# Kernel tuning notes

Hardware: AMD Instinct MI355X
Metric: run time of the kernel (lower is better)

The kernel has to match this reference:

```python
import jax, jax.numpy as jnp
import numpy as np

B, S, H = 32, 2048, 1024  # S == MAX_LENGTH
SIGMA = 1.0


def setup_inputs() -> dict:
    key = jax.random.key(0)
    k1, k2, k3, k4 = jax.random.split(key, 4)
    return {
        "encoder_outputs": jax.random.normal(k1, (B, S, H), dtype=jnp.float32),
        "decoder_hidden": jax.random.normal(k2, (B, H), dtype=jnp.float32),
        "timestep": jax.random.randint(k3, (B,), 0, S, dtype=jnp.int32),
        # 0.02 scale keeps align scores in a sane range so softmax is not saturated
        "Wa_w": jax.random.normal(k4, (H, H), dtype=jnp.float32) * 0.02,
        "Wa_b": jnp.zeros((H,), dtype=jnp.float32),
    }


def reference(encoder_outputs, decoder_hidden, timestep, Wa_w, Wa_b):
    # method='monotonic', align_method='general'
    b, s_len, h = encoder_outputs.shape

    # align 'general': scores[b,s] = dec[b] . (Wa @ enc[b,s])  (torch Linear: x @ W^T + b)
    keys = jnp.einsum('bsh,dh->bsd', encoder_outputs, Wa_w) + Wa_b  # [B,S,H]
    scores = jnp.einsum('bh,bsh->bs', decoder_hidden, keys)          # [B,S]

    # monotonic: p_t = timestep, gaussian window centered at p_t
    s = jnp.arange(s_len, dtype=jnp.float32)                          # [S]
    p_t = timestep.astype(jnp.float32)[:, None]                       # [B,1]
    gaussian = jnp.exp(-((s[None, :] - p_t) ** 2) / (2.0 * SIGMA ** 2))  # [B,S]

    attn = jax.nn.softmax(scores, axis=1) * gaussian                  # [B,S]
    context = jnp.einsum('bs,bsh->bh', attn, encoder_outputs)         # [B,H]
    return context, attn
```

## Files before the change

### kernel.cpp

```cpp
#include <hip/hip_runtime.h>

#define NB 32
#define NS 2048
#define NH 1024
#define WIN 15

__global__ __launch_bounds__(256) void k1_v(const float* __restrict__ dec,
                                            const float* __restrict__ Wa,
                                            float* __restrict__ v,
                                            double* __restrict__ denomD) {
    __shared__ float4 red4[256];
    int blk = blockIdx.x;
    int b = blk & 31, ht = blk >> 5;
    int t = threadIdx.x;
    if (blk == 0 && t < NB) denomD[t] = 0.0;

    int ds = t >> 6, hl = t & 63;
    int h = ht * 256 + hl * 4;
    const float* decb = dec + b * NH + ds * 256;
    const float* wa   = Wa + (size_t)(ds * 256) * NH + h;

    float4 accA = {0.f, 0.f, 0.f, 0.f}, accB = {0.f, 0.f, 0.f, 0.f};
#pragma unroll 4
    for (int d = 0; d < 256; d += 2) {
        float sA = decb[d];
        float sB = decb[d + 1];
        float4 wA = *(const float4*)(wa + (size_t)d * NH);
        float4 wB = *(const float4*)(wa + (size_t)(d + 1) * NH);
        accA.x = fmaf(sA, wA.x, accA.x); accA.y = fmaf(sA, wA.y, accA.y);
        accA.z = fmaf(sA, wA.z, accA.z); accA.w = fmaf(sA, wA.w, accA.w);
        accB.x = fmaf(sB, wB.x, accB.x); accB.y = fmaf(sB, wB.y, accB.y);
        accB.z = fmaf(sB, wB.z, accB.z); accB.w = fmaf(sB, wB.w, accB.w);
    }
    float4 acc = {accA.x + accB.x, accA.y + accB.y, accA.z + accB.z, accA.w + accB.w};
    red4[t] = acc;
    __syncthreads();
    if (t < 64) {
        float4 r0 = red4[t], r1 = red4[t + 64], r2 = red4[t + 128], r3 = red4[t + 192];
        float4 r = {r0.x + r1.x + r2.x + r3.x, r0.y + r1.y + r2.y + r3.y,
                    r0.z + r1.z + r2.z + r3.z, r0.w + r1.w + r2.w + r3.w};
        *(float4*)(v + b * NH + ht * 256 + t * 4) = r;
    }
}

__global__ __launch_bounds__(512) void k2_scores(const float* __restrict__ enc,
                                                 const float* __restrict__ v,
                                                 float* __restrict__ scores,
                                                 double* __restrict__ denomD) {
    __shared__ float vs[NH];
    __shared__ float rowsc[64];
    int t = threadIdx.x, wid = t >> 6, lane = t & 63;
    int b = blockIdx.x >> 5;
    int row0 = blockIdx.x << 6;

    ((float2*)vs)[t] = ((const float2*)(v + b * NH))[t];
    __syncthreads();
    const float4* vv = (const float4*)vs;
    float4 vr0 = vv[lane], vr1 = vv[64 + lane], vr2 = vv[128 + lane], vr3 = vv[192 + lane];

#pragma unroll
    for (int tile = 0; tile < 2; ++tile) {
        int r0 = row0 + tile * 32 + wid * 4;
        const float4* eb = (const float4*)(enc + (size_t)r0 * NH);
        float acc[4];
#pragma unroll
        for (int r = 0; r < 4; ++r) {
            float4 x0 = eb[r * 256 + lane];
            float4 x1 = eb[r * 256 + 64 + lane];
            float4 x2 = eb[r * 256 + 128 + lane];
            float4 x3 = eb[r * 256 + 192 + lane];
            float s = 0.f;
            s = fmaf(x0.x, vr0.x, s); s = fmaf(x0.y, vr0.y, s);
            s = fmaf(x0.z, vr0.z, s); s = fmaf(x0.w, vr0.w, s);
            s = fmaf(x1.x, vr1.x, s); s = fmaf(x1.y, vr1.y, s);
            s = fmaf(x1.z, vr1.z, s); s = fmaf(x1.w, vr1.w, s);
            s = fmaf(x2.x, vr2.x, s); s = fmaf(x2.y, vr2.y, s);
            s = fmaf(x2.z, vr2.z, s); s = fmaf(x2.w, vr2.w, s);
            s = fmaf(x3.x, vr3.x, s); s = fmaf(x3.y, vr3.y, s);
            s = fmaf(x3.z, vr3.z, s); s = fmaf(x3.w, vr3.w, s);
            acc[r] = s;
        }
#pragma unroll
        for (int r = 0; r < 4; ++r) {
#pragma unroll
            for (int off = 32; off >= 1; off >>= 1) acc[r] += __shfl_xor(acc[r], off, 64);
            if (lane == 0) {
                scores[r0 + r] = acc[r];
                rowsc[tile * 32 + wid * 4 + r] = acc[r];
            }
        }
    }
    __syncthreads();
    if (t < 64) {
        double e = exp((double)rowsc[t]);
#pragma unroll
        for (int off = 32; off >= 1; off >>= 1) e += __shfl_xor(e, off, 64);
        if (t == 0) atomicAdd(&denomD[b], e);
    }
}

__global__ __launch_bounds__(256) void k3_out(const float* __restrict__ enc,
                                              const float* __restrict__ scores,
                                              const int* __restrict__ ts,
                                              const double* __restrict__ denomD,
                                              float* __restrict__ ctx,
                                              float* __restrict__ attn) {
    __shared__ float wv[32];
    int b = blockIdx.x >> 3;
    int c = blockIdx.x & 7;
    int t = threadIdx.x;

    float lse = (float)log(denomD[b]);
    int p = ts[b];
    float pf = (float)p;

    int s = c * 256 + t;
    float sc = scores[b * NS + s];
    float d = (float)s - pf;
    attn[(size_t)b * NS + s] = expf(sc - lse - 0.5f * d * d);

    if ((p >> 8) == c) {
        int w0 = max(0, p - WIN), w1 = min(NS - 1, p + WIN);
        const float* sb = scores + (size_t)b * NS;
        if (t < 32) {
            int r = w0 + t;
            float w = 0.f;
            if (r <= w1) {
                float dr = (float)r - pf;
                w = expf(sb[r] - lse - 0.5f * dr * dr);
            }
            wv[t] = w;
        }
        __syncthreads();
        const float* eb = enc + (size_t)b * NS * NH;
        float a0 = 0.f, a1 = 0.f, a2 = 0.f, a3 = 0.f;
#pragma unroll 8
        for (int r = 0; r < 32; ++r) {
            float w = wv[r];
            const float* er = eb + (size_t)min(w0 + r, NS - 1) * NH;
            a0 = fmaf(w, er[t],       a0);
            a1 = fmaf(w, er[t + 256], a1);
            a2 = fmaf(w, er[t + 512], a2);
            a3 = fmaf(w, er[t + 768], a3);
        }
        ctx[b * NH + t]       = a0;
        ctx[b * NH + t + 256] = a1;
        ctx[b * NH + t + 512] = a2;
        ctx[b * NH + t + 768] = a3;
    }
}

extern "C" void kernel_launch(void* const* d_in, const int* in_sizes, int n_in,
                              void* d_out, int out_size, void* d_ws, size_t ws_size,
                              hipStream_t stream) {
    const float* enc  = (const float*)d_in[0];
    const float* dec  = (const float*)d_in[1];
    const int*   ts   = (const int*)d_in[2];
    const float* Wa_w = (const float*)d_in[3];

    float* out  = (float*)d_out;
    float* ctx  = out;
    float* attn = out + NB * NH;

    float*  v      = (float*)d_ws;
    float*  scores = v + NB * NH;
    double* denomD = (double*)(scores + NB * NS);

    k1_v     <<<128,  256, 0, stream>>>(dec, Wa_w, v, denomD);
    k2_scores<<<1024, 512, 0, stream>>>(enc, v, scores, denomD);
    k3_out   <<<NB*8, 256, 0, stream>>>(enc, scores, ts, denomD, ctx, attn);
}
```

Before: 66.87 us.

## Stage encoder rows into LDS with async global_load_lds double buffering

Rewrites the score kernel so each wave streams its 8 encoder rows through a per-wave double-buffered LDS area using direct global-to-LDS loads, computing one row's dot product while the next is in flight. The vector v is now read straight from global memory into registers instead of through shared memory. The goal is to overlap HBM fetches with the dot products and shuffle reductions on this memory-bound pass. In exchange, only one row is prefetched per wave, where the old code issued four rows of loads at once, and the 64 KB LDS footprint per block limits how many blocks can share a CU.

```diff
diff --git a/kernel.cpp b/kernel.cpp
--- a/kernel.cpp
+++ b/kernel.cpp
@@ -43,52 +43,63 @@
     }
 }
 
+__device__ __forceinline__ void stage_row(const float* g, float* l) {
+    __builtin_amdgcn_global_load_lds((const __attribute__((address_space(1))) void*)g,
+                                     (__attribute__((address_space(3))) void*)l, 16, 0, 0);
+    __builtin_amdgcn_global_load_lds((const __attribute__((address_space(1))) void*)(g + 256),
+                                     (__attribute__((address_space(3))) void*)(l + 256), 16, 0, 0);
+    __builtin_amdgcn_global_load_lds((const __attribute__((address_space(1))) void*)(g + 512),
+                                     (__attribute__((address_space(3))) void*)(l + 512), 16, 0, 0);
+    __builtin_amdgcn_global_load_lds((const __attribute__((address_space(1))) void*)(g + 768),
+                                     (__attribute__((address_space(3))) void*)(l + 768), 16, 0, 0);
+}
+
 __global__ __launch_bounds__(512) void k2_scores(const float* __restrict__ enc,
                                                  const float* __restrict__ v,
                                                  float* __restrict__ scores,
                                                  double* __restrict__ denomD) {
-    __shared__ float vs[NH];
+    __shared__ float buf[8][2][NH];
     __shared__ float rowsc[64];
-    int t = threadIdx.x, wid = t >> 6, lane = t & 63;
+    int t = threadIdx.x, w = t >> 6, lane = t & 63;
     int b = blockIdx.x >> 5;
-    int row0 = blockIdx.x << 6;
+    int wrow0 = (blockIdx.x << 6) + w * 8;
+    const float* g0 = enc + (size_t)wrow0 * NH + lane * 4;
 
-    ((float2*)vs)[t] = ((const float2*)(v + b * NH))[t];
-    __syncthreads();
-    const float4* vv = (const float4*)vs;
-    float4 vr0 = vv[lane], vr1 = vv[64 + lane], vr2 = vv[128 + lane], vr3 = vv[192 + lane];
+    const float4* vb = (const float4*)(v + b * NH);
+    float4 vr0 = vb[lane], vr1 = vb[64 + lane], vr2 = vb[128 + lane], vr3 = vb[192 + lane];
+    asm volatile("s_waitcnt vmcnt(0)" ::: "memory");
 
+    stage_row(g0, &buf[w][0][0]);
+
+    float* sl0 = &buf[w][0][0];
+    float* sl1 = &buf[w][1][0];
+
+    for (int i = 0; i < 8; ++i) {
+        __builtin_amdgcn_sched_barrier(0);
+        if (i < 7) {
+            stage_row(g0 + (size_t)(i + 1) * NH, (i & 1) ? sl0 : sl1);
+            asm volatile("s_waitcnt vmcnt(4)" ::: "memory");
+        } else {
+            asm volatile("s_waitcnt vmcnt(0)" ::: "memory");
+        }
+        __builtin_amdgcn_sched_barrier(0);
+        const float4* fb = (const float4*)((i & 1) ? sl1 : sl0);
+        float4 x0 = fb[lane];
+        float4 x1 = fb[64 + lane];
+        float4 x2 = fb[128 + lane];
+        float4 x3 = fb[192 + lane];
+        float s = 0.f;
+        s = fmaf(x0.x, vr0.x, s); s = fmaf(x0.y, vr0.y, s);
+        s = fmaf(x0.z, vr0.z, s); s = fmaf(x0.w, vr0.w, s);
+        s = fmaf(x1.x, vr1.x, s); s = fmaf(x1.y, vr1.y, s);
+        s = fmaf(x1.z, vr1.z, s); s = fmaf(x1.w, vr1.w, s);
+        s = fmaf(x2.x, vr2.x, s); s = fmaf(x2.y, vr2.y, s);
+        s = fmaf(x2.z, vr2.z, s); s = fmaf(x2.w, vr2.w, s);
+        s = fmaf(x3.x, vr3.x, s); s = fmaf(x3.y, vr3.y, s);
+        s = fmaf(x3.z, vr3.z, s); s = fmaf(x3.w, vr3.w, s);
 #pragma unroll
-    for (int tile = 0; tile < 2; ++tile) {
-        int r0 = row0 + tile * 32 + wid * 4;
-        const float4* eb = (const float4*)(enc + (size_t)r0 * NH);
-        float acc[4];
-#pragma unroll
-        for (int r = 0; r < 4; ++r) {
-            float4 x0 = eb[r * 256 + lane];
-            float4 x1 = eb[r * 256 + 64 + lane];
-            float4 x2 = eb[r * 256 + 128 + lane];
-            float4 x3 = eb[r * 256 + 192 + lane];
-            float s = 0.f;
-            s = fmaf(x0.x, vr0.x, s); s = fmaf(x0.y, vr0.y, s);
-            s = fmaf(x0.z, vr0.z, s); s = fmaf(x0.w, vr0.w, s);
-            s = fmaf(x1.x, vr1.x, s); s = fmaf(x1.y, vr1.y, s);
-            s = fmaf(x1.z, vr1.z, s); s = fmaf(x1.w, vr1.w, s);
-            s = fmaf(x2.x, vr2.x, s); s = fmaf(x2.y, vr2.y, s);
-            s = fmaf(x2.z, vr2.z, s); s = fmaf(x2.w, vr2.w, s);
-            s = fmaf(x3.x, vr3.x, s); s = fmaf(x3.y, vr3.y, s);
-            s = fmaf(x3.z, vr3.z, s); s = fmaf(x3.w, vr3.w, s);
-            acc[r] = s;
-        }
-#pragma unroll
-        for (int r = 0; r < 4; ++r) {
-#pragma unroll
-            for (int off = 32; off >= 1; off >>= 1) acc[r] += __shfl_xor(acc[r], off, 64);
-            if (lane == 0) {
-                scores[r0 + r] = acc[r];
-                rowsc[tile * 32 + wid * 4 + r] = acc[r];
-            }
-        }
+        for (int off = 32; off >= 1; off >>= 1) s += __shfl_xor(s, off, 64);
+        if (lane == 0) { scores[wrow0 + i] = s; rowsc[w * 8 + i] = s; }
     }
     __syncthreads();
     if (t < 64) {
```

Result: slower. 70.52 us (+5.5%).
